# Kernel tuning notes

Hardware: AMD Instinct MI355X
Metric: run time of the kernel (lower is better)

Reference implementation:

```python
import jax, jax.numpy as jnp
import numpy as np
import math

B, L, D, H, DK, DV = 4, 1024, 1024, 16, 64, 64


def setup_inputs() -> dict:
    key0 = jax.random.key(0)
    ks = jax.random.split(key0, 12)
    s = 0.02
    return {
        "key":   jax.random.normal(ks[0], (B, L, D), jnp.float32),
        "value": jax.random.normal(ks[1], (B, L, D), jnp.float32),
        "query": jax.random.normal(ks[2], (B, L, D), jnp.float32),
        "mask":  jax.random.randint(ks[3], (B, L, L), 0, 2).astype(bool),
        "Wq": jax.random.normal(ks[4], (D, H * DK), jnp.float32) * s,
        "bq": jnp.zeros((H * DK,), jnp.float32),
        "Wk": jax.random.normal(ks[5], (D, H * DK), jnp.float32) * s,
        "bk": jnp.zeros((H * DK,), jnp.float32),
        "Wv": jax.random.normal(ks[6], (D, H * DV), jnp.float32) * s,
        "bv": jnp.zeros((H * DV,), jnp.float32),
        "Wo": jax.random.normal(ks[7], (H * DV, D), jnp.float32) * s,
        "bo": jnp.zeros((D,), jnp.float32),
    }


def _shape(x, d):
    # (B, L, H*d) -> (B, H, L, d)
    b, l, _ = x.shape
    return x.reshape(b, l, H, d).transpose(0, 2, 1, 3)


def reference(key, value, query, mask, Wq, bq, Wk, bk, Wv, bv, Wo, bo):
    k = _shape(key @ Wk + bk, DK)       # (B,H,L,DK)
    v = _shape(value @ Wv + bv, DV)     # (B,H,L,DV)
    q = _shape(query @ Wq + bq, DK) / math.sqrt(DK)
    scores = jnp.einsum("bhqd,bhkd->bhqk", q, k)  # (B,H,L,L) fp32
    scores = jnp.where(mask[:, None, :, :], jnp.float32(-1e18), scores)
    # coverage (training path, step=None): triangular cumulative penalty
    maxes = jnp.max(scores, axis=3, keepdims=True)
    exp_score = jnp.exp(scores - maxes)
    # tril-ones matmul over exp_score[:, :, :-1, :] == cumsum along query axis
    penalty_body = jnp.cumsum(exp_score[:, :, :-1, :], axis=2)
    no_penalty = jnp.ones_like(penalty_body[:, :, :1, :])
    penalty = jnp.concatenate([no_penalty, penalty_body], axis=2)
    unnorm = exp_score / (penalty + 1e-8)
    attn = unnorm / jnp.sum(unnorm, axis=3, keepdims=True)
    context = jnp.einsum("bhqk,bhkd->bhqd", attn, v)  # (B,H,L,DV)
    context = context.transpose(0, 2, 1, 3).reshape(B, L, H * DV)
    final_output = context @ Wo + bo  # (B,L,D)
    return final_output
```

## Files before the change

### kernel.cpp

```cpp
#include <hip/hip_runtime.h>
#include <hip/hip_bf16.h>


typedef unsigned short u16;
typedef unsigned int u32;
typedef __bf16 v8bf __attribute__((ext_vector_type(8)));
typedef u16    v8us __attribute__((ext_vector_type(8)));
typedef float  v4f  __attribute__((ext_vector_type(4)));

__device__ __forceinline__ u16 f2b(float f){
  __hip_bfloat16 h = __float2bfloat16(f);
  return __builtin_bit_cast(u16, h);
}

__global__ void detect_kernel(const u32* __restrict__ m, int* __restrict__ flag){
  __shared__ int sb1, sb3, snz;
  int tid = threadIdx.x;
  if (tid == 0){ sb1 = 0; sb3 = 0; snz = 0; }
  __syncthreads();
  int l1 = 0, l3 = 0, ln = 0;
  for (int i = tid; i < 65536; i += 256){
    u32 v = m[i];
    u32 b1 = (v >> 8) & 0xffu, b2 = (v >> 16) & 0xffu, b3 = (v >> 24) & 0xffu;
    l1 |= (b1 == 0x3fu);
    l3 |= (b3 == 0x3fu);
    ln |= ((b1 | b2 | b3) != 0u);
  }
  if (l1) atomicOr(&sb1, 1);
  if (l3) atomicOr(&sb3, 1);
  if (ln) atomicOr(&snz, 1);
  __syncthreads();
  if (tid == 0) *flag = sb1 ? 3 : (sb3 ? 2 : (snz ? 0 : 1));
}

__global__ __launch_bounds__(256)
void pack_mask(const void* __restrict__ m, const int* __restrict__ modep,
               u32* __restrict__ bm)
{
  const int w = blockIdx.x * 256 + threadIdx.x;
  const int mode = *modep;
  u32 out = 0;
  if (mode == 0){
    const u32* p = (const u32*)m + (size_t)w * 8;
    #pragma unroll
    for (int i = 0; i < 8; i++){
      u32 v = p[i];
      if (v & 0x000000ffu) out |= 1u << (4*i+0);
      if (v & 0x0000ff00u) out |= 1u << (4*i+1);
      if (v & 0x00ff0000u) out |= 1u << (4*i+2);
      if (v & 0xff000000u) out |= 1u << (4*i+3);
    }
  } else if (mode == 3){
    const u16* p = (const u16*)m + (size_t)w * 32;
    for (int i = 0; i < 32; i++) if (p[i]) out |= 1u << i;
  } else {
    const u32* p = (const u32*)m + (size_t)w * 32;
    for (int i = 0; i < 32; i++) if (p[i]) out |= 1u << i;
  }
  bm[w] = out;
}

__global__ __launch_bounds__(256)
void cast_bf16(const float* __restrict__ in, u16* __restrict__ out){
  const int i = blockIdx.x * 256 + threadIdx.x;
  const float4* p = (const float4*)(in + (size_t)i * 8);
  float4 a = p[0], b = p[1];
  v8us r;
  r[0]=f2b(a.x); r[1]=f2b(a.y); r[2]=f2b(a.z); r[3]=f2b(a.w);
  r[4]=f2b(b.x); r[5]=f2b(b.y); r[6]=f2b(b.z); r[7]=f2b(b.w);
  ((v8us*)out)[i] = r;
}

__global__ __launch_bounds__(256)
void transpose_cast(const float* __restrict__ W, u16* __restrict__ Wt){
  __shared__ float T[64][65];
  const int ki = blockIdx.y, ni = blockIdx.x, t = threadIdx.x;
  const int r = t >> 2, c4 = (t & 3) * 16;
  const float4* src = (const float4*)&W[(size_t)(ki*64 + r) * 1024 + ni*64 + c4];
  #pragma unroll
  for (int i = 0; i < 4; i++){
    float4 f = src[i];
    T[r][c4+4*i+0]=f.x; T[r][c4+4*i+1]=f.y; T[r][c4+4*i+2]=f.z; T[r][c4+4*i+3]=f.w;
  }
  __syncthreads();
  u16* dst = &Wt[(size_t)(ni*64 + r) * 1024 + ki*64 + c4];
  v8us o0, o1;
  #pragma unroll
  for (int j = 0; j < 8; j++){ o0[j] = f2b(T[c4+j][r]); o1[j] = f2b(T[c4+8+j][r]); }
  *(v8us*)dst = o0;
  *(v8us*)(dst + 8) = o1;
}

template<int OMODE>
__global__ __launch_bounds__(256)
void gemm_bf16(const u16* __restrict__ A, const u16* __restrict__ Wt,
               const float* __restrict__ bias, float scale, void* __restrict__ outp)
{
  __shared__ alignas(16) u16 As[128][72];
  __shared__ alignas(16) u16 Bs[64][72];
  const int tid = threadIdx.x, l = tid & 63, w = tid >> 6;
  const int li = l & 15, g = l >> 4;
  const int rowBase = blockIdx.y * 128, colBase = blockIdx.x * 64;

  v4f acc[2][4];
  #pragma unroll
  for (int i = 0; i < 2; i++)
    #pragma unroll
    for (int j = 0; j < 4; j++) acc[i][j] = (v4f){0.f,0.f,0.f,0.f};

  const int ar = tid >> 1, ak = (tid & 1) * 32;
  const int br = tid >> 2, bk = (tid & 3) * 16;

  for (int kt = 0; kt < 16; ++kt){
    const int k0 = kt * 64;
    __syncthreads();
    {
      const v8us* as = (const v8us*)&A[(size_t)(rowBase + ar) * 1024 + k0 + ak];
      v8us a0 = as[0], a1 = as[1], a2 = as[2], a3 = as[3];
      *(v8us*)&As[ar][ak]      = a0;
      *(v8us*)&As[ar][ak + 8]  = a1;
      *(v8us*)&As[ar][ak + 16] = a2;
      *(v8us*)&As[ar][ak + 24] = a3;
      const v8us* bs = (const v8us*)&Wt[(size_t)(colBase + br) * 1024 + k0 + bk];
      v8us b0 = bs[0], b1 = bs[1];
      *(v8us*)&Bs[br][bk]     = b0;
      *(v8us*)&Bs[br][bk + 8] = b1;
    }
    __syncthreads();
    #pragma unroll
    for (int kk = 0; kk < 2; ++kk){
      v8bf af[2], bf[4];
      #pragma unroll
      for (int mt = 0; mt < 2; ++mt)
        af[mt] = *(const v8bf*)&As[w*32 + mt*16 + li][kk*32 + g*8];
      #pragma unroll
      for (int nt = 0; nt < 4; ++nt)
        bf[nt] = *(const v8bf*)&Bs[nt*16 + li][kk*32 + g*8];
      #pragma unroll
      for (int mt = 0; mt < 2; ++mt)
        #pragma unroll
        for (int nt = 0; nt < 4; ++nt)
          acc[mt][nt] = __builtin_amdgcn_mfma_f32_16x16x32_bf16(af[mt], bf[nt], acc[mt][nt], 0, 0, 0);
    }
  }

  #pragma unroll
  for (int mt = 0; mt < 2; ++mt){
    #pragma unroll
    for (int nt = 0; nt < 4; ++nt){
      const int gc = colBase + nt*16 + li;
      const float bs = bias[gc];
      #pragma unroll
      for (int r = 0; r < 4; ++r){
        const int gr = rowBase + w*32 + mt*16 + g*4 + r;
        float v = acc[mt][nt][r] + bs;
        if (OMODE == 0){
          v *= scale;
          const int bb = gr >> 10, lp = gr & 1023;
          const int h = gc >> 6, dk = gc & 63;
          ((u16*)outp)[((((size_t)bb*16 + h) << 10) + lp) * 64 + dk] = f2b(v);
        } else {
          ((float*)outp)[(size_t)gr * 1024 + gc] = v;
        }
      }
    }
  }
}

__global__ __launch_bounds__(256)
void rowmax_kernel(const u16* __restrict__ Qb, const u16* __restrict__ Kb,
                   const u32* __restrict__ bm, float* __restrict__ mbuf)
{
  const int tid = threadIdx.x, l = tid & 63, w = tid >> 6;
  const int li = l & 15, g = l >> 4;
  const int bid = blockIdx.x;
  const int bh = bid >> 4, qb = bid & 15;
  const int b = bh >> 4;
  const int qrow0 = qb * 64 + w * 16;
  const u32* bmb = bm + ((size_t)b << 15);

  const u16* qbase = &Qb[((size_t)bh * 1024 + qrow0 + li) * 64 + g * 8];
  const v8bf a0 = *(const v8bf*)qbase;
  const v8bf a1 = *(const v8bf*)(qbase + 32);

  float rm[4] = {-3.0e38f, -3.0e38f, -3.0e38f, -3.0e38f};

  for (int kt = 0; kt < 64; ++kt){
    const u16* kbase = &Kb[((size_t)bh * 1024 + kt*16 + li) * 64 + g * 8];
    v8bf b0 = *(const v8bf*)kbase;
    v8bf b1 = *(const v8bf*)(kbase + 32);
    v4f s = (v4f){0.f,0.f,0.f,0.f};
    s = __builtin_amdgcn_mfma_f32_16x16x32_bf16(a0, b0, s, 0, 0, 0);
    s = __builtin_amdgcn_mfma_f32_16x16x32_bf16(a1, b1, s, 0, 0, 0);
    const int bit = ((kt & 1) << 4) + li;
    #pragma unroll
    for (int r = 0; r < 4; ++r){
      const int row = qrow0 + g*4 + r;
      const u32 mw = bmb[(row << 5) | (kt >> 1)];
      const float sv = ((mw >> bit) & 1u) ? -1e18f : s[r];
      rm[r] = fmaxf(rm[r], sv);
    }
  }
  #pragma unroll
  for (int r = 0; r < 4; ++r){
    float v = rm[r];
    v = fmaxf(v, __shfl_xor(v, 1));
    v = fmaxf(v, __shfl_xor(v, 2));
    v = fmaxf(v, __shfl_xor(v, 4));
    v = fmaxf(v, __shfl_xor(v, 8));
    rm[r] = v;
  }
  if (li == 0){
    #pragma unroll
    for (int r = 0; r < 4; ++r)
      mbuf[(size_t)bh * 1024 + qrow0 + g*4 + r] = rm[r];
  }
}

__global__ __launch_bounds__(256)
void colsum_kernel(const u16* __restrict__ Qb, const u16* __restrict__ Kb,
                   const u32* __restrict__ bm, const float* __restrict__ mbuf,
                   float* __restrict__ Tsum)
{
  __shared__ float Tw[4][256];
  const int tid = threadIdx.x, l = tid & 63, w = tid >> 6;
  const int li = l & 15, g = l >> 4;
  const int bid = blockIdx.x;
  const int bh = bid >> 6, qc = (bid >> 2) & 15, kb = bid & 3;
  const int b = bh >> 4;
  const int col0 = kb * 256;
  const int qrow0 = qc * 64 + w * 16;
  const u32* bmb = bm + ((size_t)b << 15);

  const u16* qbase = &Qb[((size_t)bh * 1024 + qrow0 + li) * 64 + g * 8];
  const v8bf a0 = *(const v8bf*)qbase;
  const v8bf a1 = *(const v8bf*)(qbase + 32);
  float mrow[4];
  #pragma unroll
  for (int r = 0; r < 4; ++r) mrow[r] = mbuf[(size_t)bh * 1024 + qrow0 + g*4 + r];

  #pragma unroll
  for (int nt = 0; nt < 16; ++nt){
    const u16* kbase = &Kb[((size_t)bh * 1024 + col0 + nt*16 + li) * 64 + g * 8];
    v8bf b0 = *(const v8bf*)kbase;
    v8bf b1 = *(const v8bf*)(kbase + 32);
    v4f s = (v4f){0.f,0.f,0.f,0.f};
    s = __builtin_amdgcn_mfma_f32_16x16x32_bf16(a0, b0, s, 0, 0, 0);
    s = __builtin_amdgcn_mfma_f32_16x16x32_bf16(a1, b1, s, 0, 0, 0);
    const int wi = (col0 >> 5) + (nt >> 1);
    const int bit = ((nt & 1) << 4) + li;
    float t = 0.f;
    #pragma unroll
    for (int r = 0; r < 4; ++r){
      const int row = qrow0 + g*4 + r;
      const u32 mw = bmb[(row << 5) | wi];
      const float e = ((mw >> bit) & 1u) ? 0.f : __expf(s[r] - mrow[r]);
      t += e;
    }
    t += __shfl_xor(t, 16);
    t += __shfl_xor(t, 32);
    if (g == 0) Tw[w][nt*16 + li] = t;
  }
  __syncthreads();
  const float s4 = Tw[0][tid&255] + Tw[1][tid&255] + Tw[2][tid&255] + Tw[3][tid&255];
  Tsum[(((size_t)bh * 16 + qc) << 10) + col0 + (tid & 255)] = s4;
}

__global__ __launch_bounds__(256)
void scan_kernel(const float* __restrict__ Tsum, float* __restrict__ Cscan){
  const int bid = blockIdx.x;
  const int bh = bid >> 2, cg = bid & 3;
  const int col = cg * 256 + threadIdx.x;
  float run = 0.f;
  for (int qc = 0; qc < 16; ++qc){
    const size_t idx = (((size_t)bh * 16 + qc) << 10) + col;
    Cscan[idx] = run;
    run += Tsum[idx];
  }
}

__global__ __launch_bounds__(256)
void attn2_kernel(const u16* __restrict__ Qb, const u16* __restrict__ Kb,
                  const u16* __restrict__ Vb, const u32* __restrict__ bm,
                  const float* __restrict__ mbuf, const float* __restrict__ Cscan,
                  u16* __restrict__ ctxb)
{
  __shared__ alignas(16) u16 Vt[64][264];
  __shared__ alignas(16) u16 Ulds[4][16][264];
  __shared__ float Tw[4][256];

  const int tid = threadIdx.x, l = tid & 63, w = tid >> 6;
  const int li = l & 15, g = l >> 4;
  const int bid = blockIdx.x;
  const int bh = bid >> 4, qc = bid & 15;
  const int b = bh >> 4, h = bh & 15;
  const int qrow0 = qc * 64 + w * 16;
  const u32* bmb = bm + ((size_t)b << 15);

  const u16* qbase = &Qb[((size_t)bh * 1024 + qrow0 + li) * 64 + g * 8];
  const v8bf a0 = *(const v8bf*)qbase;
  const v8bf a1 = *(const v8bf*)(qbase + 32);
  float mrow[4];
  #pragma unroll
  for (int r = 0; r < 4; ++r) mrow[r] = mbuf[(size_t)bh * 1024 + qrow0 + g*4 + r];

  v4f pv[4];
  #pragma unroll
  for (int n = 0; n < 4; ++n) pv[n] = (v4f){0.f,0.f,0.f,0.f};
  float rs[4] = {0.f, 0.f, 0.f, 0.f};

  for (int kb = 0; kb < 4; ++kb){
    const int col0 = kb * 256;
    if (kb) __syncthreads();

    #pragma unroll
    for (int j = 0; j < 8; ++j){
      const int k = (tid >> 3) + j * 32;
      const int dv0 = (tid & 7) * 8;
      v8us vv = *(const v8us*)&Vb[((size_t)bh * 1024 + col0 + k) * 64 + dv0];
      #pragma unroll
      for (int i = 0; i < 8; ++i) Vt[dv0 + i][k] = vv[i];
    }

    v4f sc[16];
    float cg16[16];
    #pragma unroll
    for (int nt = 0; nt < 16; ++nt){
      const u16* kbase = &Kb[((size_t)bh * 1024 + col0 + nt*16 + li) * 64 + g * 8];
      v8bf b0 = *(const v8bf*)kbase;
      v8bf b1 = *(const v8bf*)(kbase + 32);
      v4f s = (v4f){0.f,0.f,0.f,0.f};
      s = __builtin_amdgcn_mfma_f32_16x16x32_bf16(a0, b0, s, 0, 0, 0);
      s = __builtin_amdgcn_mfma_f32_16x16x32_bf16(a1, b1, s, 0, 0, 0);
      const int wi = (col0 >> 5) + (nt >> 1);
      const int bit = ((nt & 1) << 4) + li;
      float t = 0.f;
      #pragma unroll
      for (int r = 0; r < 4; ++r){
        const int row = qrow0 + g*4 + r;
        const u32 mw = bmb[(row << 5) | wi];
        const float e = ((mw >> bit) & 1u) ? 0.f : __expf(s[r] - mrow[r]);
        s[r] = e;
        t += e;
      }
      sc[nt] = s;
      const float t1 = __shfl_up(t, 16);
      const float t2 = __shfl_up(t, 32);
      const float t3 = __shfl_up(t, 48);
      float c = 0.f;
      if (g >= 1) c += t1;
      if (g >= 2) c += t2;
      if (g >= 3) c += t3;
      cg16[nt] = c;
      if (g == 3) Tw[w][nt*16 + li] = c + t;
    }
    __syncthreads();

    #pragma unroll
    for (int nt = 0; nt < 16; ++nt){
      const int c = nt*16 + li;
      float base = Cscan[(((size_t)bh * 16 + qc) << 10) + col0 + c];
      if (w > 0) base += Tw[0][c];
      if (w > 1) base += Tw[1][c];
      if (w > 2) base += Tw[2][c];
      float run = 0.f;
      #pragma unroll
      for (int r = 0; r < 4; ++r){
        const int Rg = qrow0 + g*4 + r;
        float pen = base + cg16[nt] + run;
        if (Rg == 0) pen = 1.0f;
        const float e = sc[nt][r];
        const float u = e / (pen + 1e-8f);
        run += e;
        rs[r] += u;
        Ulds[w][g*4 + r][c] = f2b(u);
      }
    }

    #pragma unroll
    for (int kk = 0; kk < 8; ++kk){
      v8bf ua = *(const v8bf*)&Ulds[w][li][g*8 + kk*32];
      #pragma unroll
      for (int n = 0; n < 4; ++n){
        v8bf vb = *(const v8bf*)&Vt[n*16 + li][g*8 + kk*32];
        pv[n] = __builtin_amdgcn_mfma_f32_16x16x32_bf16(ua, vb, pv[n], 0, 0, 0);
      }
    }
  }

  #pragma unroll
  for (int r = 0; r < 4; ++r){
    float v = rs[r];
    v += __shfl_xor(v, 1);
    v += __shfl_xor(v, 2);
    v += __shfl_xor(v, 4);
    v += __shfl_xor(v, 8);
    rs[r] = v;
  }

  #pragma unroll
  for (int n = 0; n < 4; ++n){
    #pragma unroll
    for (int r = 0; r < 4; ++r){
      const int lrow = qrow0 + g*4 + r;
      const int dv = n*16 + li;
      ctxb[(((size_t)b << 10) + lrow) * 1024 + h*64 + dv] = f2b(pv[n][r] / rs[r]);
    }
  }
}

extern "C" void kernel_launch(void* const* d_in, const int* in_sizes, int n_in,
                              void* d_out, int out_size, void* d_ws, size_t ws_size,
                              hipStream_t stream)
{
  const float* key   = (const float*)d_in[0];
  const float* value = (const float*)d_in[1];
  const float* query = (const float*)d_in[2];
  const void*  mask  = d_in[3];
  const float* Wq = (const float*)d_in[4];
  const float* bq = (const float*)d_in[5];
  const float* Wk = (const float*)d_in[6];
  const float* bk = (const float*)d_in[7];
  const float* Wv = (const float*)d_in[8];
  const float* bv = (const float*)d_in[9];
  const float* Wo = (const float*)d_in[10];
  const float* bo = (const float*)d_in[11];

  if (ws_size < (58ull << 20)) return;

  char* ws = (char*)d_ws;
  u16*   Qb    = (u16*)(ws);
  u16*   Kb    = (u16*)(ws + (8ull  << 20));
  u16*   Vb    = (u16*)(ws + (16ull << 20));
  u16*   Ac    = (u16*)(ws + (24ull << 20));
  u16*   ctxb  = (u16*)(ws + (32ull << 20));
  u16*   Wtq   = (u16*)(ws + (40ull << 20));
  u16*   Wtk   = (u16*)(ws + (42ull << 20));
  u16*   Wtv   = (u16*)(ws + (44ull << 20));
  u16*   Wto   = (u16*)(ws + (46ull << 20));
  float* mbuf  = (float*)(ws + (48ull << 20));
  u32*   bmp   = (u32*)  (ws + (48ull << 20) + (256u << 10));
  int*   flag  = (int*)  (ws + (48ull << 20) + (768u << 10));
  float* Tsum  = (float*)(ws + (49ull << 20));
  float* Cscan = (float*)(ws + (53ull << 20));

  detect_kernel<<<1, 256, 0, stream>>>((const u32*)mask, flag);
  pack_mask<<<512, 256, 0, stream>>>(mask, flag, bmp);

  dim3 tg(16, 16);
  transpose_cast<<<tg, 256, 0, stream>>>(Wq, Wtq);
  transpose_cast<<<tg, 256, 0, stream>>>(Wk, Wtk);
  transpose_cast<<<tg, 256, 0, stream>>>(Wv, Wtv);
  transpose_cast<<<tg, 256, 0, stream>>>(Wo, Wto);

  dim3 gg(16, 32);
  cast_bf16<<<2048, 256, 0, stream>>>(query, Ac);
  gemm_bf16<0><<<gg, 256, 0, stream>>>(Ac, Wtq, bq, 0.125f, Qb);
  cast_bf16<<<2048, 256, 0, stream>>>(key, Ac);
  gemm_bf16<0><<<gg, 256, 0, stream>>>(Ac, Wtk, bk, 1.0f, Kb);
  cast_bf16<<<2048, 256, 0, stream>>>(value, Ac);
  gemm_bf16<0><<<gg, 256, 0, stream>>>(Ac, Wtv, bv, 1.0f, Vb);

  rowmax_kernel<<<1024, 256, 0, stream>>>(Qb, Kb, bmp, mbuf);
  colsum_kernel<<<4096, 256, 0, stream>>>(Qb, Kb, bmp, mbuf, Tsum);
  scan_kernel<<<256, 256, 0, stream>>>(Tsum, Cscan);
  attn2_kernel<<<1024, 256, 0, stream>>>(Qb, Kb, Vb, bmp, mbuf, Cscan, ctxb);

  gemm_bf16<1><<<gg, 256, 0, stream>>>(ctxb, Wto, bo, 1.0f, d_out);
}
```

Before: 541.5 us.

## Use direct global-to-LDS loads with XOR swizzle in GEMM; shrink attention key tile

The projection GEMMs now stage A and W tiles through global_load_lds with an XOR-swizzled LDS layout, and each wave computes a 64x32 output tile instead of 32x64. This removes the register round-trip and the padded LDS layout, and aims to cut bank conflicts and VGPR use. The attention kernel now processes 128-key chunks instead of 256, with launch bounds requesting 4 blocks per CU to raise occupancy, at the cost of twice as many barriers and V transposes per block. The penalty division becomes a hardware reciprocal multiply, which is slightly less accurate.

```diff
diff --git a/kernel.cpp b/kernel.cpp
--- a/kernel.cpp
+++ b/kernel.cpp
@@ -93,66 +93,78 @@
 
 template<int OMODE>
 __global__ __launch_bounds__(256)
-void gemm_bf16(const u16* __restrict__ A, const u16* __restrict__ Wt,
-               const float* __restrict__ bias, float scale, void* __restrict__ outp)
-{
-  __shared__ alignas(16) u16 As[128][72];
-  __shared__ alignas(16) u16 Bs[64][72];
+void gemm_gl(const u16* __restrict__ A, const u16* __restrict__ Wt,
+             const float* __restrict__ bias, float scale, void* __restrict__ outp)
+{
+  __shared__ alignas(16) u16 As[128 * 64];
+  __shared__ alignas(16) u16 Bs[64 * 64];
   const int tid = threadIdx.x, l = tid & 63, w = tid >> 6;
   const int li = l & 15, g = l >> 4;
   const int rowBase = blockIdx.y * 128, colBase = blockIdx.x * 64;
-
-  v4f acc[2][4];
-  #pragma unroll
-  for (int i = 0; i < 2; i++)
-    #pragma unroll
-    for (int j = 0; j < 4; j++) acc[i][j] = (v4f){0.f,0.f,0.f,0.f};
-
-  const int ar = tid >> 1, ak = (tid & 1) * 32;
-  const int br = tid >> 2, bk = (tid & 3) * 16;
+  const int wm = w >> 1, wn = w & 1;
+
+  v4f acc[4][2];
+  #pragma unroll
+  for (int i = 0; i < 4; i++)
+    #pragma unroll
+    for (int j = 0; j < 2; j++) acc[i][j] = (v4f){0.f,0.f,0.f,0.f};
 
   for (int kt = 0; kt < 16; ++kt){
     const int k0 = kt * 64;
     __syncthreads();
-    {
-      const v8us* as = (const v8us*)&A[(size_t)(rowBase + ar) * 1024 + k0 + ak];
-      v8us a0 = as[0], a1 = as[1], a2 = as[2], a3 = as[3];
-      *(v8us*)&As[ar][ak]      = a0;
-      *(v8us*)&As[ar][ak + 8]  = a1;
-      *(v8us*)&As[ar][ak + 16] = a2;
-      *(v8us*)&As[ar][ak + 24] = a3;
-      const v8us* bs = (const v8us*)&Wt[(size_t)(colBase + br) * 1024 + k0 + bk];
-      v8us b0 = bs[0], b1 = bs[1];
-      *(v8us*)&Bs[br][bk]     = b0;
-      *(v8us*)&Bs[br][bk + 8] = b1;
+    #pragma unroll
+    for (int j = 0; j < 4; ++j){
+      const int s = j * 256 + tid;
+      const int r = s >> 3, c8 = s & 7;
+      const int c8s = c8 ^ (r & 7);
+      const u16* src = &A[(size_t)(rowBase + r) * 1024 + k0 + c8s * 8];
+      __builtin_amdgcn_global_load_lds(
+        (const __attribute__((address_space(1))) void*)src,
+        (__attribute__((address_space(3))) void*)(As + (size_t)(j*256 + w*64) * 8),
+        16, 0, 0);
+    }
+    #pragma unroll
+    for (int j = 0; j < 2; ++j){
+      const int s = j * 256 + tid;
+      const int r = s >> 3, c8 = s & 7;
+      const int c8s = c8 ^ (r & 7);
+      const u16* src = &Wt[(size_t)(colBase + r) * 1024 + k0 + c8s * 8];
+      __builtin_amdgcn_global_load_lds(
+        (const __attribute__((address_space(1))) void*)src,
+        (__attribute__((address_space(3))) void*)(Bs + (size_t)(j*256 + w*64) * 8),
+        16, 0, 0);
     }
     __syncthreads();
     #pragma unroll
     for (int kk = 0; kk < 2; ++kk){
-      v8bf af[2], bf[4];
-      #pragma unroll
-      for (int mt = 0; mt < 2; ++mt)
-        af[mt] = *(const v8bf*)&As[w*32 + mt*16 + li][kk*32 + g*8];
-      #pragma unroll
-      for (int nt = 0; nt < 4; ++nt)
-        bf[nt] = *(const v8bf*)&Bs[nt*16 + li][kk*32 + g*8];
-      #pragma unroll
-      for (int mt = 0; mt < 2; ++mt)
+      v8bf af[4], bf[2];
+      #pragma unroll
+      for (int mt = 0; mt < 4; ++mt){
+        const int r = wm*64 + mt*16 + li;
+        af[mt] = *(const v8bf*)&As[r*64 + (((kk*4 + g) ^ (r & 7)) * 8)];
+      }
+      #pragma unroll
+      for (int nt = 0; nt < 2; ++nt){
+        const int c = wn*32 + nt*16 + li;
+        bf[nt] = *(const v8bf*)&Bs[c*64 + (((kk*4 + g) ^ (c & 7)) * 8)];
+      }
+      #pragma unroll
+      for (int mt = 0; mt < 4; ++mt)
         #pragma unroll
-        for (int nt = 0; nt < 4; ++nt)
+        for (int nt = 0; nt < 2; ++nt)
           acc[mt][nt] = __builtin_amdgcn_mfma_f32_16x16x32_bf16(af[mt], bf[nt], acc[mt][nt], 0, 0, 0);
     }
   }
 
   #pragma unroll
-  for (int mt = 0; mt < 2; ++mt){
-    #pragma unroll
-    for (int nt = 0; nt < 4; ++nt){
-      const int gc = colBase + nt*16 + li;
+  for (int mt = 0; mt < 4; ++mt){
+    #pragma unroll
+    for (int nt = 0; nt < 2; ++nt){
+      const int gc = colBase + wn*32 + nt*16 + li;
       const float bs = bias[gc];
       #pragma unroll
       for (int r = 0; r < 4; ++r){
-        const int gr = rowBase + w*32 + mt*16 + g*4 + r;
+        const int gr = rowBase + wm*64 + mt*16 + g*4 + r;
         float v = acc[mt][nt][r] + bs;
         if (OMODE == 0){
           v *= scale;
@@ -279,15 +291,15 @@
   }
 }
 
-__global__ __launch_bounds__(256)
+__global__ __launch_bounds__(256, 4)
 void attn2_kernel(const u16* __restrict__ Qb, const u16* __restrict__ Kb,
                   const u16* __restrict__ Vb, const u32* __restrict__ bm,
                   const float* __restrict__ mbuf, const float* __restrict__ Cscan,
                   u16* __restrict__ ctxb)
 {
-  __shared__ alignas(16) u16 Vt[64][264];
-  __shared__ alignas(16) u16 Ulds[4][16][264];
-  __shared__ float Tw[4][256];
+  __shared__ alignas(16) u16 Vt[64][136];
+  __shared__ alignas(16) u16 Ulds[4][16][136];
+  __shared__ float Tw[4][128];
 
   const int tid = threadIdx.x, l = tid & 63, w = tid >> 6;
   const int li = l & 15, g = l >> 4;
@@ -309,12 +321,12 @@
   for (int n = 0; n < 4; ++n) pv[n] = (v4f){0.f,0.f,0.f,0.f};
   float rs[4] = {0.f, 0.f, 0.f, 0.f};
 
-  for (int kb = 0; kb < 4; ++kb){
-    const int col0 = kb * 256;
+  for (int kb = 0; kb < 8; ++kb){
+    const int col0 = kb * 128;
     if (kb) __syncthreads();
 
     #pragma unroll
-    for (int j = 0; j < 8; ++j){
+    for (int j = 0; j < 4; ++j){
       const int k = (tid >> 3) + j * 32;
       const int dv0 = (tid & 7) * 8;
       v8us vv = *(const v8us*)&Vb[((size_t)bh * 1024 + col0 + k) * 64 + dv0];
@@ -322,10 +334,10 @@
       for (int i = 0; i < 8; ++i) Vt[dv0 + i][k] = vv[i];
     }
 
-    v4f sc[16];
-    float cg16[16];
-    #pragma unroll
-    for (int nt = 0; nt < 16; ++nt){
+    v4f sc[8];
+    float cg16[8];
+    #pragma unroll
+    for (int nt = 0; nt < 8; ++nt){
       const u16* kbase = &Kb[((size_t)bh * 1024 + col0 + nt*16 + li) * 64 + g * 8];
       v8bf b0 = *(const v8bf*)kbase;
       v8bf b1 = *(const v8bf*)(kbase + 32);
@@ -357,7 +369,7 @@
     __syncthreads();
 
     #pragma unroll
-    for (int nt = 0; nt < 16; ++nt){
+    for (int nt = 0; nt < 8; ++nt){
       const int c = nt*16 + li;
       float base = Cscan[(((size_t)bh * 16 + qc) << 10) + col0 + c];
       if (w > 0) base += Tw[0][c];
@@ -370,7 +382,7 @@
         float pen = base + cg16[nt] + run;
         if (Rg == 0) pen = 1.0f;
         const float e = sc[nt][r];
-        const float u = e / (pen + 1e-8f);
+        const float u = e * __builtin_amdgcn_rcpf(pen + 1e-8f);
         run += e;
         rs[r] += u;
         Ulds[w][g*4 + r][c] = f2b(u);
@@ -378,7 +390,7 @@
     }
 
     #pragma unroll
-    for (int kk = 0; kk < 8; ++kk){
+    for (int kk = 0; kk < 4; ++kk){
       v8bf ua = *(const v8bf*)&Ulds[w][li][g*8 + kk*32];
       #pragma unroll
       for (int n = 0; n < 4; ++n){
@@ -455,16 +467,16 @@
 
   dim3 gg(16, 32);
   cast_bf16<<<2048, 256, 0, stream>>>(query, Ac);
-  gemm_bf16<0><<<gg, 256, 0, stream>>>(Ac, Wtq, bq, 0.125f, Qb);
+  gemm_gl<0><<<gg, 256, 0, stream>>>(Ac, Wtq, bq, 0.125f, Qb);
   cast_bf16<<<2048, 256, 0, stream>>>(key, Ac);
-  gemm_bf16<0><<<gg, 256, 0, stream>>>(Ac, Wtk, bk, 1.0f, Kb);
+  gemm_gl<0><<<gg, 256, 0, stream>>>(Ac, Wtk, bk, 1.0f, Kb);
   cast_bf16<<<2048, 256, 0, stream>>>(value, Ac);
-  gemm_bf16<0><<<gg, 256, 0, stream>>>(Ac, Wtv, bv, 1.0f, Vb);
+  gemm_gl<0><<<gg, 256, 0, stream>>>(Ac, Wtv, bv, 1.0f, Vb);
 
   rowmax_kernel<<<1024, 256, 0, stream>>>(Qb, Kb, bmp, mbuf);
   colsum_kernel<<<4096, 256, 0, stream>>>(Qb, Kb, bmp, mbuf, Tsum);
   scan_kernel<<<256, 256, 0, stream>>>(Tsum, Cscan);
   attn2_kernel<<<1024, 256, 0, stream>>>(Qb, Kb, Vb, bmp, mbuf, Cscan, ctxb);
 
-  gemm_bf16<1><<<gg, 256, 0, stream>>>(ctxb, Wto, bo, 1.0f, d_out);
-}
+  gemm_gl<1><<<gg, 256, 0, stream>>>(ctxb, Wto, bo, 1.0f, d_out);
+}
```

Measured after the change: 499.6 us. 1.08x faster.
